# Kernel tuning notes

Measured on AMD Instinct MI355X. Metric: run time of the kernel, lower is better.

The kernel has to match this reference:

```python
import jax, jax.numpy as jnp
import numpy as np

EPS = 1e-12
B, S, H, NH, L, F = 8, 512, 768, 12, 12, 3072
V, TV, P = 21128, 2, 512
DH = H // NH


def layer_norm(x, g, b):
    m = jnp.mean(x, axis=-1, keepdims=True)
    v = jnp.var(x, axis=-1, keepdims=True)
    return g * (x - m) / jnp.sqrt(v + EPS) + b


def setup_inputs() -> dict:
    key = jax.random.key(0)
    ks = iter(jax.random.split(key, 40))
    r = lambda shape: (jax.random.normal(next(ks), shape, jnp.float32) * 0.02)
    inp = {
        "input_ids": jax.random.randint(next(ks), (B, S), 0, V, jnp.int32),
        "segment_ids": jax.random.randint(next(ks), (B, S), 0, TV, jnp.int32),
        "attention_mask": jnp.ones((B, 1, 1, S), jnp.float32),
        "tok_emb": r((V, H)),
        "pos_emb": r((P, H)),
        "type_emb": r((TV, H)),
        "emb_g": jnp.ones((H,), jnp.float32),
        "emb_b": jnp.zeros((H,), jnp.float32),
        # stacked per-layer params [L, ...]
        "Wq": r((L, H, H)), "bq": jnp.zeros((L, H), jnp.float32),
        "Wk": r((L, H, H)), "bk": jnp.zeros((L, H), jnp.float32),
        "Wv": r((L, H, H)), "bv": jnp.zeros((L, H), jnp.float32),
        "Wao": r((L, H, H)), "bao": jnp.zeros((L, H), jnp.float32),
        "ln1_g": jnp.ones((L, H), jnp.float32), "ln1_b": jnp.zeros((L, H), jnp.float32),
        "Wi": r((L, H, F)), "bi": jnp.zeros((L, F), jnp.float32),
        "Wio": r((L, F, H)), "bio": jnp.zeros((L, H), jnp.float32),
        "ln2_g": jnp.ones((L, H), jnp.float32), "ln2_b": jnp.zeros((L, H), jnp.float32),
    }
    return inp


def reference(input_ids, segment_ids, attention_mask,
              tok_emb, pos_emb, type_emb, emb_g, emb_b,
              Wq, bq, Wk, bk, Wv, bv, Wao, bao, ln1_g, ln1_b,
              Wi, bi, Wio, bio, ln2_g, ln2_b):
    # ---- embedding: token + type + position, then LayerNorm ----
    x = tok_emb[input_ids] + type_emb[segment_ids] + pos_emb[None, :S, :]
    x = layer_norm(x, emb_g, emb_b)  # [B,S,H]

    mask_add = (1.0 - attention_mask) * -10000.0  # [B,1,1,S]
    scale = 1.0 / jnp.sqrt(jnp.asarray(DH, x.dtype))

    def split_heads(t):  # [B,S,H] -> [B,NH,S,DH]
        return t.reshape(B, S, NH, DH).transpose(0, 2, 1, 3)

    for l in range(Wq.shape[0]):
        q = split_heads(x @ Wq[l] + bq[l])
        k = split_heads(x @ Wk[l] + bk[l])
        v = split_heads(x @ Wv[l] + bv[l])
        score = jnp.einsum("bhqd,bhkd->bhqk", q, k) * scale + mask_add
        attn = jax.nn.softmax(score, axis=-1)
        ctx = jnp.einsum("bhqk,bhkd->bhqd", attn, v)
        ctx = ctx.transpose(0, 2, 1, 3).reshape(B, S, H)
        # attention output: dense + residual + LN
        attn_out = layer_norm(ctx @ Wao[l] + bao[l] + x, ln1_g[l], ln1_b[l])
        # FFN: dense-gelu-dense + residual + LN (exact erf gelu as in tf.keras)
        h = jax.nn.gelu(attn_out @ Wi[l] + bi[l], approximate=False)
        x = layer_norm(h @ Wio[l] + bio[l] + attn_out, ln2_g[l], ln2_b[l])

    return x  # sequence output [B,S,H]
```

## Files before the change

kernel.cpp:

```cpp
#include <hip/hip_runtime.h>
#include <math.h>

static constexpr int Bc = 8;
static constexpr int Sc = 512;
static constexpr int Hc = 768;
static constexpr int NHc = 12;
static constexpr int Lc = 12;
static constexpr int Fc = 3072;
static constexpr int DHc = 64;
static constexpr int NTOK = Bc * Sc;
static constexpr int QKVN = 3 * Hc;

static constexpr size_t W_QKV_OFF = 0;
static constexpr size_t W_AO_OFF  = 1769472;
static constexpr size_t W_I_OFF   = 2359296;
static constexpr size_t W_IO_OFF  = 4718592;
static constexpr size_t LW        = 7077888;

typedef _Float16 h16x8 __attribute__((ext_vector_type(8)));
typedef float f32x4 __attribute__((ext_vector_type(4)));
typedef unsigned short us4 __attribute__((ext_vector_type(4)));
typedef unsigned short us8 __attribute__((ext_vector_type(8)));
typedef unsigned int u32x4 __attribute__((ext_vector_type(4)));

__device__ __forceinline__ unsigned short f2h(float f) {
    _Float16 h = (_Float16)f;
    return __builtin_bit_cast(unsigned short, h);
}

#define AS1 __attribute__((address_space(1)))
#define AS3 __attribute__((address_space(3)))
__device__ __forceinline__ void gld_lds16(const void* g, void* l) {
    __builtin_amdgcn_global_load_lds((const AS1 void*)g, (AS3 void*)l, 16, 0, 0);
}

__global__ __launch_bounds__(256) void prep_kernel(
    const float* __restrict__ Wq, const float* __restrict__ Wk,
    const float* __restrict__ Wv, const float* __restrict__ Wao,
    const float* __restrict__ Wi, const float* __restrict__ Wio,
    const float* __restrict__ bq, const float* __restrict__ bk,
    const float* __restrict__ bv, unsigned short* __restrict__ WALL,
    float* __restrict__ BALL)
{
    int t = blockIdx.x, l = blockIdx.y;
    int tid = threadIdx.x;

    if (t >= 1728) {
        int idx = (t - 1728) * 256 + tid;
        float v = (idx < 768) ? bq[l * Hc + idx]
                : (idx < 1536) ? bk[l * Hc + idx - 768]
                               : bv[l * Hc + idx - 1536];
        BALL[(size_t)l * QKVN + idx] = v;
        return;
    }

    const float* src;
    unsigned short* dst;
    int K, N, ntn, local;
    if (t < 576) {
        int mat = t / 144; local = t % 144;
        K = 768; N = 768; ntn = 12;
        src = (mat == 0 ? Wq : mat == 1 ? Wk : mat == 2 ? Wv : Wao) + (size_t)l * 589824;
        dst = WALL + (size_t)l * LW + (mat < 3 ? (size_t)mat * 589824 : W_AO_OFF);
    } else if (t < 1152) {
        local = t - 576; K = 768; N = 3072; ntn = 48;
        src = Wi + (size_t)l * 2359296;
        dst = WALL + (size_t)l * LW + W_I_OFF;
    } else {
        local = t - 1152; K = 3072; N = 768; ntn = 12;
        src = Wio + (size_t)l * 2359296;
        dst = WALL + (size_t)l * LW + W_IO_OFF;
    }
    int n0 = (local % ntn) * 64, k0 = (local / ntn) * 64;

    __shared__ float tl[64][65];
    int tx = tid & 15, ty = tid >> 4;
#pragma unroll
    for (int j = 0; j < 4; j++) {
        int k = ty + j * 16;
        float4 v = *(const float4*)(src + (size_t)(k0 + k) * N + n0 + tx * 4);
        tl[k][tx * 4 + 0] = v.x; tl[k][tx * 4 + 1] = v.y;
        tl[k][tx * 4 + 2] = v.z; tl[k][tx * 4 + 3] = v.w;
    }
    __syncthreads();
#pragma unroll
    for (int q = 0; q < 2; q++) {
        int chunk = q * 256 + tid;
        int row = chunk >> 3, c = chunk & 7;
        us8 o;
#pragma unroll
        for (int j = 0; j < 8; j++) o[j] = f2h(tl[c * 8 + j][row]);
        *(us8*)(dst + (size_t)(n0 + row) * K + k0 + c * 8) = o;
    }
}

__global__ __launch_bounds__(256) void embed_ln_kernel(
    const int* __restrict__ ids, const int* __restrict__ seg,
    const float* __restrict__ tok, const float* __restrict__ typ,
    const float* __restrict__ pos, const float* __restrict__ g,
    const float* __restrict__ b, float* __restrict__ outf,
    unsigned short* __restrict__ outb)
{
    int t = blockIdx.x;
    int si = t % Sc;
    int id = ids[t], sg = seg[t];
    const float* tp = tok + (size_t)id * Hc;
    const float* yp = typ + (size_t)sg * Hc;
    const float* pp = pos + (size_t)si * Hc;

    float e[3];
    float s = 0.f, s2 = 0.f;
#pragma unroll
    for (int j = 0; j < 3; j++) {
        int h = threadIdx.x + j * 256;
        float v = tp[h] + yp[h] + pp[h];
        e[j] = v; s += v; s2 += v * v;
    }
    __shared__ float red[8];
#pragma unroll
    for (int o = 32; o > 0; o >>= 1) { s += __shfl_xor(s, o); s2 += __shfl_xor(s2, o); }
    int lane = threadIdx.x & 63, wid = threadIdx.x >> 6;
    if (lane == 0) { red[wid] = s; red[4 + wid] = s2; }
    __syncthreads();
    if (threadIdx.x == 0) {
        red[0] = red[0] + red[1] + red[2] + red[3];
        red[4] = red[4] + red[5] + red[6] + red[7];
    }
    __syncthreads();
    float mean = red[0] * (1.0f / Hc);
    float var  = red[4] * (1.0f / Hc) - mean * mean;
    float rstd = rsqrtf(var + 1e-12f);
    float* op = outf + (size_t)t * Hc;
    unsigned short* ob = outb + (size_t)t * Hc;
#pragma unroll
    for (int j = 0; j < 3; j++) {
        int h = threadIdx.x + j * 256;
        float v = g[h] * (e[j] - mean) * rstd + b[h];
        op[h] = v;
        ob[h] = f2h(v);
    }
}

__global__ __launch_bounds__(256) void add_ln_kernel(
    const unsigned short* __restrict__ tin, const float* __restrict__ res,
    const float* __restrict__ g, const float* __restrict__ b,
    float* __restrict__ outf, unsigned short* __restrict__ outb)
{
    int t = blockIdx.x;
    const unsigned short* ip = tin + (size_t)t * Hc;
    const float* rp = res + (size_t)t * Hc;

    float e[3];
    float s = 0.f, s2 = 0.f;
#pragma unroll
    for (int j = 0; j < 3; j++) {
        int h = threadIdx.x + j * 256;
        float v = (float)__builtin_bit_cast(_Float16, ip[h]) + rp[h];
        e[j] = v; s += v; s2 += v * v;
    }
    __shared__ float red[8];
#pragma unroll
    for (int o = 32; o > 0; o >>= 1) { s += __shfl_xor(s, o); s2 += __shfl_xor(s2, o); }
    int lane = threadIdx.x & 63, wid = threadIdx.x >> 6;
    if (lane == 0) { red[wid] = s; red[4 + wid] = s2; }
    __syncthreads();
    if (threadIdx.x == 0) {
        red[0] = red[0] + red[1] + red[2] + red[3];
        red[4] = red[4] + red[5] + red[6] + red[7];
    }
    __syncthreads();
    float mean = red[0] * (1.0f / Hc);
    float var  = red[4] * (1.0f / Hc) - mean * mean;
    float rstd = rsqrtf(var + 1e-12f);
    float* op = outf + (size_t)t * Hc;
    unsigned short* ob = outb + (size_t)t * Hc;
#pragma unroll
    for (int j = 0; j < 3; j++) {
        int h = threadIdx.x + j * 256;
        float v = g[h] * (e[j] - mean) * rstd + b[h];
        op[h] = v;
        ob[h] = f2h(v);
    }
}

__global__ __launch_bounds__(256) void add_ln2f_kernel(
    const float* __restrict__ t0, const float* __restrict__ t1,
    const float* __restrict__ res, const float* __restrict__ g,
    const float* __restrict__ b, float* __restrict__ outf,
    unsigned short* __restrict__ outb)
{
    int t = blockIdx.x;
    const float* i0 = t0 + (size_t)t * Hc;
    const float* i1 = t1 + (size_t)t * Hc;
    const float* rp = res + (size_t)t * Hc;

    float e[3];
    float s = 0.f, s2 = 0.f;
#pragma unroll
    for (int j = 0; j < 3; j++) {
        int h = threadIdx.x + j * 256;
        float v = i0[h] + i1[h] + rp[h];
        e[j] = v; s += v; s2 += v * v;
    }
    __shared__ float red[8];
#pragma unroll
    for (int o = 32; o > 0; o >>= 1) { s += __shfl_xor(s, o); s2 += __shfl_xor(s2, o); }
    int lane = threadIdx.x & 63, wid = threadIdx.x >> 6;
    if (lane == 0) { red[wid] = s; red[4 + wid] = s2; }
    __syncthreads();
    if (threadIdx.x == 0) {
        red[0] = red[0] + red[1] + red[2] + red[3];
        red[4] = red[4] + red[5] + red[6] + red[7];
    }
    __syncthreads();
    float mean = red[0] * (1.0f / Hc);
    float var  = red[4] * (1.0f / Hc) - mean * mean;
    float rstd = rsqrtf(var + 1e-12f);
    float* op = outf + (size_t)t * Hc;
    unsigned short* ob = outb + (size_t)t * Hc;
#pragma unroll
    for (int j = 0; j < 3; j++) {
        int h = threadIdx.x + j * 256;
        float v = g[h] * (e[j] - mean) * rstd + b[h];
        op[h] = v;
        ob[h] = f2h(v);
    }
}

template <int OUT>
__global__ __launch_bounds__(256) void gemm_mfma(
    const unsigned short* __restrict__ A,
    const unsigned short* __restrict__ Bt,
    const float* __restrict__ bias,
    unsigned short* __restrict__ Cb,
    unsigned short* __restrict__ VTp,
    float* __restrict__ Cf,
    int M, int N, int K, int kspan)
{
    __shared__ __align__(16) unsigned short As[128 * 64];
    __shared__ __align__(16) unsigned short Bs[128 * 64];

    int tid = threadIdx.x;
    int l = tid & 63, w = tid >> 6;
    int m0 = blockIdx.x * 128, n0 = blockIdx.y * 128;
    int lr = l & 15;
    int kg = l >> 4;
    int wr = (w >> 1) * 64, wc = (w & 1) * 64;
    int lx = lr & 7;
    int kbeg = blockIdx.z * kspan;

    f32x4 acc[4][4] = {};

    for (int k0 = kbeg; k0 < kbeg + kspan; k0 += 64) {
#pragma unroll
        for (int p = 0; p < 4; p++) {
            int i = p * 256 + w * 64 + l;
            int row = i >> 3;
            int slot = (i & 7) ^ (row & 7);
            const unsigned short* ga = A + (size_t)(m0 + row) * K + k0 + slot * 8;
            const unsigned short* gb = Bt + (size_t)(n0 + row) * K + k0 + slot * 8;
            unsigned short* la = As + (size_t)(p * 256 + w * 64) * 8;
            unsigned short* lb = Bs + (size_t)(p * 256 + w * 64) * 8;
            gld_lds16(ga, la);
            gld_lds16(gb, lb);
        }
        asm volatile("s_waitcnt vmcnt(0)" ::: "memory");
        __syncthreads();

#pragma unroll
        for (int kh = 0; kh < 2; kh++) {
            h16x8 av[4], bv[4];
#pragma unroll
            for (int f = 0; f < 4; f++) {
                int sl = (kh * 4 + kg) ^ lx;
                av[f] = *(const h16x8*)(As + (wr + f * 16 + lr) * 64 + sl * 8);
                bv[f] = *(const h16x8*)(Bs + (wc + f * 16 + lr) * 64 + sl * 8);
            }
#pragma unroll
            for (int i = 0; i < 4; i++)
#pragma unroll
                for (int j = 0; j < 4; j++)
                    acc[i][j] = __builtin_amdgcn_mfma_f32_16x16x32_f16(
                        av[i], bv[j], acc[i][j], 0, 0, 0);
        }
        __syncthreads();
    }

#pragma unroll
    for (int i = 0; i < 4; i++) {
        int rbase = m0 + wr + i * 16 + kg * 4;
#pragma unroll
        for (int j = 0; j < 4; j++) {
            int col = n0 + wc + j * 16 + lr;
            float bcol = (OUT == 4 && blockIdx.z > 0) ? 0.f : bias[col];
            if (OUT == 3 && col >= 1536) {
                int vcol = col - 1536;
                int hh = vcol >> 6, d = vcol & 63;
                int bbb = rbase >> 9, s0 = rbase & 511;
                us4 ob;
#pragma unroll
                for (int r = 0; r < 4; r++) ob[r] = f2h(acc[i][j][r] + bcol);
                *(us4*)(VTp + ((((size_t)bbb * NHc + hh) * DHc + d) << 9) + s0) = ob;
            } else if (OUT == 4) {
                float* op = Cf + (size_t)blockIdx.z * M * N;
#pragma unroll
                for (int r = 0; r < 4; r++)
                    op[(size_t)(rbase + r) * N + col] = acc[i][j][r] + bcol;
            } else {
                int ldc = (OUT == 3) ? 1536 : N;
#pragma unroll
                for (int r = 0; r < 4; r++) {
                    float v = acc[i][j][r] + bcol;
                    if (OUT == 1) v = 0.5f * v * (1.0f + erff(v * 0.70710678118654752f));
                    Cb[(size_t)(rbase + r) * ldc + col] = f2h(v);
                }
            }
        }
    }
}

__global__ __launch_bounds__(256) void attn_mfma(
    const unsigned short* __restrict__ QK, const unsigned short* __restrict__ VT,
    const float* __restrict__ mask, unsigned short* __restrict__ O)
{
    const int LD = 1536;
    __shared__ __align__(16) unsigned short Ks[64 * 64];
    __shared__ __align__(16) unsigned short Vt[64 * 64];
    __shared__ float Ml[64];

    int tid = threadIdx.x;
    int l = tid & 63, w = tid >> 6;
    int g = l >> 4, c = l & 15;
    int q0 = blockIdx.x * 64;
    int h = blockIdx.y, bb = blockIdx.z;

    const size_t rowQ = (size_t)(bb * Sc + q0 + w * 16 + c) * LD + h * DHc;
    h16x8 qv[2];
    qv[0] = *(const h16x8*)(QK + rowQ + 8 * g);
    qv[1] = *(const h16x8*)(QK + rowQ + 32 + 8 * g);

    float m_run = -1e30f, l_run = 0.f;
    f32x4 acc_o[4] = {};
    const float scale = 0.125f;

    for (int kt = 0; kt < Sc; kt += 64) {
        const unsigned short* Kgb = QK + (size_t)(bb * Sc + kt) * LD + Hc + h * DHc;
#pragma unroll
        for (int p = 0; p < 2; p++) {
            int i = p * 256 + tid;
            int row = i >> 3;
            int slot = (i & 7) ^ (row & 7);
            gld_lds16(Kgb + (size_t)row * LD + slot * 8, Ks + (size_t)(p * 256 + w * 64) * 8);
        }
        const unsigned short* Vg = VT + (((size_t)bb * NHc + h) * DHc << 9) + kt;
#pragma unroll
        for (int p = 0; p < 2; p++) {
            int i = p * 256 + tid;
            int row = i >> 3;
            int slot = (i & 7) ^ (row & 7);
            gld_lds16(Vg + ((size_t)row << 9) + slot * 8, Vt + (size_t)(p * 256 + w * 64) * 8);
        }
        if (tid < 64) Ml[tid] = (1.0f - mask[bb * Sc + kt + tid]) * -10000.0f;
        asm volatile("s_waitcnt vmcnt(0)" ::: "memory");
        __syncthreads();

        f32x4 s[4] = {};
#pragma unroll
        for (int kh = 0; kh < 2; kh++) {
#pragma unroll
            for (int f = 0; f < 4; f++) {
                int row = f * 16 + c;
                h16x8 av = *(const h16x8*)(Ks + row * 64 + (((kh * 4 + g) ^ (row & 7)) * 8));
                s[f] = __builtin_amdgcn_mfma_f32_16x16x32_f16(av, qv[kh], s[f], 0, 0, 0);
            }
        }

        f32x4 mv[4];
#pragma unroll
        for (int f = 0; f < 4; f++) mv[f] = *(const f32x4*)&Ml[f * 16 + 4 * g];
        float mx = -1e30f;
#pragma unroll
        for (int f = 0; f < 4; f++)
#pragma unroll
            for (int r = 0; r < 4; r++) {
                float sv = s[f][r] * scale + mv[f][r];
                s[f][r] = sv;
                mx = fmaxf(mx, sv);
            }
        mx = fmaxf(mx, __shfl_xor(mx, 16));
        mx = fmaxf(mx, __shfl_xor(mx, 32));
        float mn = fmaxf(m_run, mx);
        float fs = __expf(m_run - mn);
        m_run = mn;
        float ps = 0.f;
        f32x4 p[4];
#pragma unroll
        for (int f = 0; f < 4; f++)
#pragma unroll
            for (int r = 0; r < 4; r++) {
                float pv = __expf(s[f][r] - mn);
                p[f][r] = pv;
                ps += pv;
            }
        ps += __shfl_xor(ps, 16);
        ps += __shfl_xor(ps, 32);
        l_run = l_run * fs + ps;
#pragma unroll
        for (int fm = 0; fm < 4; fm++)
#pragma unroll
            for (int r = 0; r < 4; r++) acc_o[fm][r] *= fs;

        unsigned pk[4][2];
#pragma unroll
        for (int f = 0; f < 4; f++)
#pragma unroll
            for (int rp = 0; rp < 2; rp++)
                pk[f][rp] = ((unsigned)f2h(p[f][2 * rp + 1]) << 16) | f2h(p[f][2 * rp]);

#pragma unroll
        for (int kh = 0; kh < 2; kh++) {
            u32x4 bw;
#pragma unroll
            for (int t = 0; t < 4; t++) {
                int srcl = (2 * ((l >> 4) & 1) + (t >> 1)) * 16 + c;
                unsigned lo = __shfl(pk[2 * kh][t & 1], srcl);
                unsigned hi = __shfl(pk[2 * kh + 1][t & 1], srcl);
                bw[t] = (g & 2) ? hi : lo;
            }
            h16x8 bfrag = __builtin_bit_cast(h16x8, bw);
#pragma unroll
            for (int fm = 0; fm < 4; fm++) {
                int row = fm * 16 + c;
                h16x8 av = *(const h16x8*)(Vt + row * 64 + (((kh * 4 + g) ^ (row & 7)) * 8));
                acc_o[fm] = __builtin_amdgcn_mfma_f32_16x16x32_f16(av, bfrag, acc_o[fm], 0, 0, 0);
            }
        }
        __syncthreads();
    }

    float rl = 1.0f / l_run;
    size_t tokrow = (size_t)(bb * Sc + q0 + w * 16 + c) * Hc + h * DHc;
#pragma unroll
    for (int fm = 0; fm < 4; fm++) {
        us4 ob;
#pragma unroll
        for (int r = 0; r < 4; r++) ob[r] = f2h(acc_o[fm][r] * rl);
        *(us4*)(O + tokrow + fm * 16 + 4 * g) = ob;
    }
}

extern "C" void kernel_launch(void* const* d_in, const int* in_sizes, int n_in,
                              void* d_out, int out_size, void* d_ws, size_t ws_size,
                              hipStream_t stream)
{
    const int*   input_ids      = (const int*)  d_in[0];
    const int*   segment_ids    = (const int*)  d_in[1];
    const float* attention_mask = (const float*)d_in[2];
    const float* tok_emb = (const float*)d_in[3];
    const float* pos_emb = (const float*)d_in[4];
    const float* type_emb= (const float*)d_in[5];
    const float* emb_g   = (const float*)d_in[6];
    const float* emb_b   = (const float*)d_in[7];
    const float* Wq  = (const float*)d_in[8];  const float* bq  = (const float*)d_in[9];
    const float* Wk  = (const float*)d_in[10]; const float* bk  = (const float*)d_in[11];
    const float* Wv  = (const float*)d_in[12]; const float* bv  = (const float*)d_in[13];
    const float* Wao = (const float*)d_in[14]; const float* bao = (const float*)d_in[15];
    const float* ln1_g = (const float*)d_in[16]; const float* ln1_b = (const float*)d_in[17];
    const float* Wi  = (const float*)d_in[18]; const float* bi  = (const float*)d_in[19];
    const float* Wio = (const float*)d_in[20]; const float* bio = (const float*)d_in[21];
    const float* ln2_g = (const float*)d_in[22]; const float* ln2_b = (const float*)d_in[23];

    float* out = (float*)d_out;

    const size_t NT = (size_t)NTOK * Hc;
    float* Xf   = (float*)d_ws;
    float* XAf  = Xf + NT;
    float* Tf01 = XAf + NT;
    float* BALL = Tf01 + 2 * NT;
    unsigned short* QKb = (unsigned short*)(BALL + (size_t)Lc * QKVN);
    unsigned short* VT  = QKb + (size_t)NTOK * 1536;
    unsigned short* Xb  = VT + NT;
    unsigned short* XAb = Xb + NT;
    unsigned short* Cb  = XAb + NT;
    unsigned short* Tb  = Cb + NT;
    unsigned short* Hb  = Tb + NT;
    unsigned short* WALL = Hb + (size_t)NTOK * Fc;

    prep_kernel<<<dim3(1737, Lc), 256, 0, stream>>>(Wq, Wk, Wv, Wao, Wi, Wio,
                                                    bq, bk, bv, WALL, BALL);

    embed_ln_kernel<<<NTOK, 256, 0, stream>>>(input_ids, segment_ids, tok_emb,
                                              type_emb, pos_emb, emb_g, emb_b, Xf, Xb);

    dim3 gQKV(NTOK / 128, QKVN / 128);
    dim3 gH(NTOK / 128, Hc / 128);
    dim3 gF(NTOK / 128, Fc / 128);
    dim3 gH2(NTOK / 128, Hc / 128, 2);
    dim3 gA(Sc / 64, NHc, Bc);

    for (int l = 0; l < Lc; l++) {
        const unsigned short* WqkvT = WALL + (size_t)l * LW + W_QKV_OFF;
        const unsigned short* WaoT  = WALL + (size_t)l * LW + W_AO_OFF;
        const unsigned short* WiT   = WALL + (size_t)l * LW + W_I_OFF;
        const unsigned short* WioT  = WALL + (size_t)l * LW + W_IO_OFF;
        const float* bqkv = BALL + (size_t)l * QKVN;

        gemm_mfma<3><<<gQKV, 256, 0, stream>>>(Xb, WqkvT, bqkv, QKb, VT, nullptr,
                                               NTOK, QKVN, Hc, Hc);
        attn_mfma<<<gA, 256, 0, stream>>>(QKb, VT, attention_mask, Cb);

        gemm_mfma<2><<<gH, 256, 0, stream>>>(Cb, WaoT, bao + (size_t)l * Hc, Tb, nullptr,
                                             nullptr, NTOK, Hc, Hc, Hc);
        add_ln_kernel<<<NTOK, 256, 0, stream>>>(Tb, Xf, ln1_g + (size_t)l * Hc,
                                                ln1_b + (size_t)l * Hc, XAf, XAb);

        gemm_mfma<1><<<gF, 256, 0, stream>>>(XAb, WiT, bi + (size_t)l * Fc, Hb, nullptr,
                                             nullptr, NTOK, Fc, Hc, Hc);
        gemm_mfma<4><<<gH2, 256, 0, stream>>>(Hb, WioT, bio + (size_t)l * Hc, nullptr,
                                              nullptr, Tf01, NTOK, Hc, Fc, Fc / 2);
        float* xout = (l == Lc - 1) ? out : Xf;
        add_ln2f_kernel<<<NTOK, 256, 0, stream>>>(Tf01, Tf01 + NT, XAf,
                                                  ln2_g + (size_t)l * Hc,
                                                  ln2_b + (size_t)l * Hc, xout, Xb);
    }
}
```

Measured before the change: 2.070 ms.

## Double-buffer GEMM LDS staging and make weight prep loop over K strips

The MFMA GEMM now double-buffers its A/B LDS tiles, issuing the global-to-LDS loads for the next K step before waiting only on the current tile, so memory latency overlaps with compute. The weight transpose/convert prep kernel is restructured so each block walks 12 consecutive 64-wide K tiles of one column strip, prefetching the next tile into registers. This uses far fewer blocks and hides load latency. Doubling the LDS footprint to 64KB per GEMM block may lower occupancy.

```diff
diff --git a/kernel.cpp b/kernel.cpp
--- a/kernel.cpp
+++ b/kernel.cpp
@@ -45,8 +45,8 @@
     int t = blockIdx.x, l = blockIdx.y;
     int tid = threadIdx.x;
 
-    if (t >= 1728) {
-        int idx = (t - 1728) * 256 + tid;
+    if (t >= 144) {
+        int idx = (t - 144) * 256 + tid;
         float v = (idx < 768) ? bq[l * Hc + idx]
                 : (idx < 1536) ? bk[l * Hc + idx - 768]
                                : bv[l * Hc + idx - 1536];
@@ -56,41 +56,57 @@
 
     const float* src;
     unsigned short* dst;
-    int K, N, ntn, local;
-    if (t < 576) {
-        int mat = t / 144; local = t % 144;
-        K = 768; N = 768; ntn = 12;
+    int K, N, n0, kbase;
+    if (t < 48) {
+        int mat = t / 12, strip = t % 12;
+        K = 768; N = 768; n0 = strip * 64; kbase = 0;
         src = (mat == 0 ? Wq : mat == 1 ? Wk : mat == 2 ? Wv : Wao) + (size_t)l * 589824;
         dst = WALL + (size_t)l * LW + (mat < 3 ? (size_t)mat * 589824 : W_AO_OFF);
-    } else if (t < 1152) {
-        local = t - 576; K = 768; N = 3072; ntn = 48;
+    } else if (t < 96) {
+        int strip = t - 48;
+        K = 768; N = 3072; n0 = strip * 64; kbase = 0;
         src = Wi + (size_t)l * 2359296;
         dst = WALL + (size_t)l * LW + W_I_OFF;
     } else {
-        local = t - 1152; K = 3072; N = 768; ntn = 12;
+        int local = t - 96;
+        int strip = local >> 2, kc = local & 3;
+        K = 3072; N = 768; n0 = strip * 64; kbase = kc * 768;
         src = Wio + (size_t)l * 2359296;
         dst = WALL + (size_t)l * LW + W_IO_OFF;
     }
-    int n0 = (local % ntn) * 64, k0 = (local / ntn) * 64;
 
     __shared__ float tl[64][65];
     int tx = tid & 15, ty = tid >> 4;
-#pragma unroll
-    for (int j = 0; j < 4; j++) {
-        int k = ty + j * 16;
-        float4 v = *(const float4*)(src + (size_t)(k0 + k) * N + n0 + tx * 4);
-        tl[k][tx * 4 + 0] = v.x; tl[k][tx * 4 + 1] = v.y;
-        tl[k][tx * 4 + 2] = v.z; tl[k][tx * 4 + 3] = v.w;
-    }
-    __syncthreads();
-#pragma unroll
-    for (int q = 0; q < 2; q++) {
-        int chunk = q * 256 + tid;
-        int row = chunk >> 3, c = chunk & 7;
-        us8 o;
-#pragma unroll
-        for (int j = 0; j < 8; j++) o[j] = f2h(tl[c * 8 + j][row]);
-        *(us8*)(dst + (size_t)(n0 + row) * K + k0 + c * 8) = o;
+
+    float4 v[4];
+#pragma unroll
+    for (int j = 0; j < 4; j++)
+        v[j] = *(const float4*)(src + (size_t)(kbase + ty + j * 16) * N + n0 + tx * 4);
+
+    for (int it = 0; it < 12; it++) {
+        int k0 = kbase + it * 64;
+#pragma unroll
+        for (int j = 0; j < 4; j++) {
+            int k = ty + j * 16;
+            tl[k][tx * 4 + 0] = v[j].x; tl[k][tx * 4 + 1] = v[j].y;
+            tl[k][tx * 4 + 2] = v[j].z; tl[k][tx * 4 + 3] = v[j].w;
+        }
+        __syncthreads();
+        if (it + 1 < 12) {
+#pragma unroll
+            for (int j = 0; j < 4; j++)
+                v[j] = *(const float4*)(src + (size_t)(k0 + 64 + ty + j * 16) * N + n0 + tx * 4);
+        }
+#pragma unroll
+        for (int q = 0; q < 2; q++) {
+            int chunk = q * 256 + tid;
+            int row = chunk >> 3, c = chunk & 7;
+            us8 o;
+#pragma unroll
+            for (int j = 0; j < 8; j++) o[j] = f2h(tl[c * 8 + j][row]);
+            *(us8*)(dst + (size_t)(n0 + row) * K + k0 + c * 8) = o;
+        }
+        __syncthreads();
     }
 }
 
@@ -237,8 +253,8 @@
     float* __restrict__ Cf,
     int M, int N, int K, int kspan)
 {
-    __shared__ __align__(16) unsigned short As[128 * 64];
-    __shared__ __align__(16) unsigned short Bs[128 * 64];
+    __shared__ __align__(16) unsigned short As[2][128 * 64];
+    __shared__ __align__(16) unsigned short Bs[2][128 * 64];
 
     int tid = threadIdx.x;
     int l = tid & 63, w = tid >> 6;
@@ -248,33 +264,47 @@
     int wr = (w >> 1) * 64, wc = (w & 1) * 64;
     int lx = lr & 7;
     int kbeg = blockIdx.z * kspan;
+    int nk = kspan / 64;
 
     f32x4 acc[4][4] = {};
 
-    for (int k0 = kbeg; k0 < kbeg + kspan; k0 += 64) {
+    auto stage = [&](int buf, int k0) {
+        unsigned short* as = &As[buf][0];
+        unsigned short* bs = &Bs[buf][0];
 #pragma unroll
         for (int p = 0; p < 4; p++) {
             int i = p * 256 + w * 64 + l;
             int row = i >> 3;
             int slot = (i & 7) ^ (row & 7);
-            const unsigned short* ga = A + (size_t)(m0 + row) * K + k0 + slot * 8;
-            const unsigned short* gb = Bt + (size_t)(n0 + row) * K + k0 + slot * 8;
-            unsigned short* la = As + (size_t)(p * 256 + w * 64) * 8;
-            unsigned short* lb = Bs + (size_t)(p * 256 + w * 64) * 8;
-            gld_lds16(ga, la);
-            gld_lds16(gb, lb);
-        }
-        asm volatile("s_waitcnt vmcnt(0)" ::: "memory");
+            gld_lds16(A + (size_t)(m0 + row) * K + k0 + slot * 8,
+                      as + (size_t)(p * 256 + w * 64) * 8);
+            gld_lds16(Bt + (size_t)(n0 + row) * K + k0 + slot * 8,
+                      bs + (size_t)(p * 256 + w * 64) * 8);
+        }
+    };
+
+    stage(0, kbeg);
+
+    for (int t = 0; t < nk; t++) {
+        int cur = t & 1;
+        if (t + 1 < nk) {
+            stage(cur ^ 1, kbeg + (t + 1) * 64);
+            asm volatile("s_waitcnt vmcnt(8)" ::: "memory");
+        } else {
+            asm volatile("s_waitcnt vmcnt(0)" ::: "memory");
+        }
         __syncthreads();
 
+        const unsigned short* as = &As[cur][0];
+        const unsigned short* bs = &Bs[cur][0];
 #pragma unroll
         for (int kh = 0; kh < 2; kh++) {
             h16x8 av[4], bv[4];
 #pragma unroll
             for (int f = 0; f < 4; f++) {
                 int sl = (kh * 4 + kg) ^ lx;
-                av[f] = *(const h16x8*)(As + (wr + f * 16 + lr) * 64 + sl * 8);
-                bv[f] = *(const h16x8*)(Bs + (wc + f * 16 + lr) * 64 + sl * 8);
+                av[f] = *(const h16x8*)(as + (wr + f * 16 + lr) * 64 + sl * 8);
+                bv[f] = *(const h16x8*)(bs + (wc + f * 16 + lr) * 64 + sl * 8);
             }
 #pragma unroll
             for (int i = 0; i < 4; i++)
@@ -486,8 +516,8 @@
     unsigned short* Hb  = Tb + NT;
     unsigned short* WALL = Hb + (size_t)NTOK * Fc;
 
-    prep_kernel<<<dim3(1737, Lc), 256, 0, stream>>>(Wq, Wk, Wv, Wao, Wi, Wio,
-                                                    bq, bk, bv, WALL, BALL);
+    prep_kernel<<<dim3(153, Lc), 256, 0, stream>>>(Wq, Wk, Wv, Wao, Wi, Wio,
+                                                   bq, bk, bv, WALL, BALL);
 
     embed_ln_kernel<<<NTOK, 256, 0, stream>>>(input_ids, segment_ids, tok_emb,
                                               type_emb, pos_emb, emb_g, emb_b, Xf, Xb);
```

After: 2.371 ms. +14.5%, slower.

## Split-K the attention-output GEMM and vectorize LayerNorm kernels to 192 threads

Applied to the files above, without the earlier changes.

The attention-output projection now uses the split-K GEMM variant (two K halves written as fp32 partials), and its residual LayerNorm reuses the two-partial add_ln2f kernel. This doubles the block count of that 768x768 GEMM for better CU occupancy, but it writes fp32 partials instead of a half-precision result, which adds memory traffic. Separately, the embedding and LayerNorm kernels are rewritten to use 192 threads, each handling one float4, with a single-barrier reduction. This cuts the loop, scalar loads and an extra sync in those kernels.

```diff
diff --git a/kernel.cpp b/kernel.cpp
--- a/kernel.cpp
+++ b/kernel.cpp
@@ -26,6 +26,9 @@
 __device__ __forceinline__ unsigned short f2h(float f) {
     _Float16 h = (_Float16)f;
     return __builtin_bit_cast(unsigned short, h);
+}
+__device__ __forceinline__ float h2f(unsigned short u) {
+    return (float)__builtin_bit_cast(_Float16, u);
 }
 
 #define AS1 __attribute__((address_space(1)))
@@ -94,7 +97,23 @@
     }
 }
 
-__global__ __launch_bounds__(256) void embed_ln_kernel(
+__device__ __forceinline__ void ln_stats192(float4 v, float& mean, float& rstd) {
+    float s = v.x + v.y + v.z + v.w;
+    float s2 = v.x * v.x + v.y * v.y + v.z * v.z + v.w * v.w;
+#pragma unroll
+    for (int o = 32; o > 0; o >>= 1) { s += __shfl_xor(s, o); s2 += __shfl_xor(s2, o); }
+    __shared__ float red[6];
+    int lane = threadIdx.x & 63, wid = threadIdx.x >> 6;
+    if (lane == 0) { red[wid] = s; red[3 + wid] = s2; }
+    __syncthreads();
+    float ts  = red[0] + red[1] + red[2];
+    float ts2 = red[3] + red[4] + red[5];
+    mean = ts * (1.0f / Hc);
+    float var = ts2 * (1.0f / Hc) - mean * mean;
+    rstd = rsqrtf(var + 1e-12f);
+}
+
+__global__ __launch_bounds__(192) void embed_ln_kernel(
     const int* __restrict__ ids, const int* __restrict__ seg,
     const float* __restrict__ tok, const float* __restrict__ typ,
     const float* __restrict__ pos, const float* __restrict__ g,
@@ -104,127 +123,52 @@
     int t = blockIdx.x;
     int si = t % Sc;
     int id = ids[t], sg = seg[t];
-    const float* tp = tok + (size_t)id * Hc;
-    const float* yp = typ + (size_t)sg * Hc;
-    const float* pp = pos + (size_t)si * Hc;
-
-    float e[3];
-    float s = 0.f, s2 = 0.f;
-#pragma unroll
-    for (int j = 0; j < 3; j++) {
-        int h = threadIdx.x + j * 256;
-        float v = tp[h] + yp[h] + pp[h];
-        e[j] = v; s += v; s2 += v * v;
-    }
-    __shared__ float red[8];
-#pragma unroll
-    for (int o = 32; o > 0; o >>= 1) { s += __shfl_xor(s, o); s2 += __shfl_xor(s2, o); }
-    int lane = threadIdx.x & 63, wid = threadIdx.x >> 6;
-    if (lane == 0) { red[wid] = s; red[4 + wid] = s2; }
-    __syncthreads();
-    if (threadIdx.x == 0) {
-        red[0] = red[0] + red[1] + red[2] + red[3];
-        red[4] = red[4] + red[5] + red[6] + red[7];
-    }
-    __syncthreads();
-    float mean = red[0] * (1.0f / Hc);
-    float var  = red[4] * (1.0f / Hc) - mean * mean;
-    float rstd = rsqrtf(var + 1e-12f);
-    float* op = outf + (size_t)t * Hc;
-    unsigned short* ob = outb + (size_t)t * Hc;
-#pragma unroll
-    for (int j = 0; j < 3; j++) {
-        int h = threadIdx.x + j * 256;
-        float v = g[h] * (e[j] - mean) * rstd + b[h];
-        op[h] = v;
-        ob[h] = f2h(v);
-    }
-}
-
-__global__ __launch_bounds__(256) void add_ln_kernel(
-    const unsigned short* __restrict__ tin, const float* __restrict__ res,
-    const float* __restrict__ g, const float* __restrict__ b,
-    float* __restrict__ outf, unsigned short* __restrict__ outb)
-{
-    int t = blockIdx.x;
-    const unsigned short* ip = tin + (size_t)t * Hc;
-    const float* rp = res + (size_t)t * Hc;
-
-    float e[3];
-    float s = 0.f, s2 = 0.f;
-#pragma unroll
-    for (int j = 0; j < 3; j++) {
-        int h = threadIdx.x + j * 256;
-        float v = (float)__builtin_bit_cast(_Float16, ip[h]) + rp[h];
-        e[j] = v; s += v; s2 += v * v;
-    }
-    __shared__ float red[8];
-#pragma unroll
-    for (int o = 32; o > 0; o >>= 1) { s += __shfl_xor(s, o); s2 += __shfl_xor(s2, o); }
-    int lane = threadIdx.x & 63, wid = threadIdx.x >> 6;
-    if (lane == 0) { red[wid] = s; red[4 + wid] = s2; }
-    __syncthreads();
-    if (threadIdx.x == 0) {
-        red[0] = red[0] + red[1] + red[2] + red[3];
-        red[4] = red[4] + red[5] + red[6] + red[7];
-    }
-    __syncthreads();
-    float mean = red[0] * (1.0f / Hc);
-    float var  = red[4] * (1.0f / Hc) - mean * mean;
-    float rstd = rsqrtf(var + 1e-12f);
-    float* op = outf + (size_t)t * Hc;
-    unsigned short* ob = outb + (size_t)t * Hc;
-#pragma unroll
-    for (int j = 0; j < 3; j++) {
-        int h = threadIdx.x + j * 256;
-        float v = g[h] * (e[j] - mean) * rstd + b[h];
-        op[h] = v;
-        ob[h] = f2h(v);
-    }
-}
-
-__global__ __launch_bounds__(256) void add_ln2f_kernel(
+    int i = threadIdx.x;
+
+    float4 tv = *(const float4*)(tok + (size_t)id * Hc + 4 * i);
+    float4 yv = *(const float4*)(typ + (size_t)sg * Hc + 4 * i);
+    float4 pv = *(const float4*)(pos + (size_t)si * Hc + 4 * i);
+    float4 v = make_float4(tv.x + yv.x + pv.x, tv.y + yv.y + pv.y,
+                           tv.z + yv.z + pv.z, tv.w + yv.w + pv.w);
+    float mean, rstd;
+    ln_stats192(v, mean, rstd);
+
+    float4 gv = *(const float4*)(g + 4 * i);
+    float4 bv = *(const float4*)(b + 4 * i);
+    float4 o = make_float4(gv.x * (v.x - mean) * rstd + bv.x,
+                           gv.y * (v.y - mean) * rstd + bv.y,
+                           gv.z * (v.z - mean) * rstd + bv.z,
+                           gv.w * (v.w - mean) * rstd + bv.w);
+    *(float4*)(outf + (size_t)t * Hc + 4 * i) = o;
+    us4 ob; ob[0] = f2h(o.x); ob[1] = f2h(o.y); ob[2] = f2h(o.z); ob[3] = f2h(o.w);
+    *(us4*)(outb + (size_t)t * Hc + 4 * i) = ob;
+}
+
+__global__ __launch_bounds__(192) void add_ln2f_kernel(
     const float* __restrict__ t0, const float* __restrict__ t1,
     const float* __restrict__ res, const float* __restrict__ g,
     const float* __restrict__ b, float* __restrict__ outf,
     unsigned short* __restrict__ outb)
 {
     int t = blockIdx.x;
-    const float* i0 = t0 + (size_t)t * Hc;
-    const float* i1 = t1 + (size_t)t * Hc;
-    const float* rp = res + (size_t)t * Hc;
-
-    float e[3];
-    float s = 0.f, s2 = 0.f;
-#pragma unroll
-    for (int j = 0; j < 3; j++) {
-        int h = threadIdx.x + j * 256;
-        float v = i0[h] + i1[h] + rp[h];
-        e[j] = v; s += v; s2 += v * v;
-    }
-    __shared__ float red[8];
-#pragma unroll
-    for (int o = 32; o > 0; o >>= 1) { s += __shfl_xor(s, o); s2 += __shfl_xor(s2, o); }
-    int lane = threadIdx.x & 63, wid = threadIdx.x >> 6;
-    if (lane == 0) { red[wid] = s; red[4 + wid] = s2; }
-    __syncthreads();
-    if (threadIdx.x == 0) {
-        red[0] = red[0] + red[1] + red[2] + red[3];
-        red[4] = red[4] + red[5] + red[6] + red[7];
-    }
-    __syncthreads();
-    float mean = red[0] * (1.0f / Hc);
-    float var  = red[4] * (1.0f / Hc) - mean * mean;
-    float rstd = rsqrtf(var + 1e-12f);
-    float* op = outf + (size_t)t * Hc;
-    unsigned short* ob = outb + (size_t)t * Hc;
-#pragma unroll
-    for (int j = 0; j < 3; j++) {
-        int h = threadIdx.x + j * 256;
-        float v = g[h] * (e[j] - mean) * rstd + b[h];
-        op[h] = v;
-        ob[h] = f2h(v);
-    }
+    int i = threadIdx.x;
+    float4 a = *(const float4*)(t0 + (size_t)t * Hc + 4 * i);
+    float4 c = *(const float4*)(t1 + (size_t)t * Hc + 4 * i);
+    float4 r = *(const float4*)(res + (size_t)t * Hc + 4 * i);
+    float4 v = make_float4(a.x + c.x + r.x, a.y + c.y + r.y,
+                           a.z + c.z + r.z, a.w + c.w + r.w);
+    float mean, rstd;
+    ln_stats192(v, mean, rstd);
+
+    float4 gv = *(const float4*)(g + 4 * i);
+    float4 bv = *(const float4*)(b + 4 * i);
+    float4 o = make_float4(gv.x * (v.x - mean) * rstd + bv.x,
+                           gv.y * (v.y - mean) * rstd + bv.y,
+                           gv.z * (v.z - mean) * rstd + bv.z,
+                           gv.w * (v.w - mean) * rstd + bv.w);
+    *(float4*)(outf + (size_t)t * Hc + 4 * i) = o;
+    us4 ob; ob[0] = f2h(o.x); ob[1] = f2h(o.y); ob[2] = f2h(o.z); ob[3] = f2h(o.w);
+    *(us4*)(outb + (size_t)t * Hc + 4 * i) = ob;
 }
 
 template <int OUT>
@@ -482,18 +426,16 @@
     unsigned short* Xb  = VT + NT;
     unsigned short* XAb = Xb + NT;
     unsigned short* Cb  = XAb + NT;
-    unsigned short* Tb  = Cb + NT;
-    unsigned short* Hb  = Tb + NT;
+    unsigned short* Hb  = Cb + NT;
     unsigned short* WALL = Hb + (size_t)NTOK * Fc;
 
     prep_kernel<<<dim3(1737, Lc), 256, 0, stream>>>(Wq, Wk, Wv, Wao, Wi, Wio,
                                                     bq, bk, bv, WALL, BALL);
 
-    embed_ln_kernel<<<NTOK, 256, 0, stream>>>(input_ids, segment_ids, tok_emb,
+    embed_ln_kernel<<<NTOK, 192, 0, stream>>>(input_ids, segment_ids, tok_emb,
                                               type_emb, pos_emb, emb_g, emb_b, Xf, Xb);
 
     dim3 gQKV(NTOK / 128, QKVN / 128);
-    dim3 gH(NTOK / 128, Hc / 128);
     dim3 gF(NTOK / 128, Fc / 128);
     dim3 gH2(NTOK / 128, Hc / 128, 2);
     dim3 gA(Sc / 64, NHc, Bc);
@@ -509,17 +451,18 @@
                                                NTOK, QKVN, Hc, Hc);
         attn_mfma<<<gA, 256, 0, stream>>>(QKb, VT, attention_mask, Cb);
 
-        gemm_mfma<2><<<gH, 256, 0, stream>>>(Cb, WaoT, bao + (size_t)l * Hc, Tb, nullptr,
-                                             nullptr, NTOK, Hc, Hc, Hc);
-        add_ln_kernel<<<NTOK, 256, 0, stream>>>(Tb, Xf, ln1_g + (size_t)l * Hc,
-                                                ln1_b + (size_t)l * Hc, XAf, XAb);
+        gemm_mfma<4><<<gH2, 256, 0, stream>>>(Cb, WaoT, bao + (size_t)l * Hc, nullptr,
+                                              nullptr, Tf01, NTOK, Hc, Hc, Hc / 2);
+        add_ln2f_kernel<<<NTOK, 192, 0, stream>>>(Tf01, Tf01 + NT, Xf,
+                                                  ln1_g + (size_t)l * Hc,
+                                                  ln1_b + (size_t)l * Hc, XAf, XAb);
 
         gemm_mfma<1><<<gF, 256, 0, stream>>>(XAb, WiT, bi + (size_t)l * Fc, Hb, nullptr,
                                              nullptr, NTOK, Fc, Hc, Hc);
         gemm_mfma<4><<<gH2, 256, 0, stream>>>(Hb, WioT, bio + (size_t)l * Hc, nullptr,
                                               nullptr, Tf01, NTOK, Hc, Fc, Fc / 2);
         float* xout = (l == Lc - 1) ? out : Xf;
-        add_ln2f_kernel<<<NTOK, 256, 0, stream>>>(Tf01, Tf01 + NT, XAf,
+        add_ln2f_kernel<<<NTOK, 192, 0, stream>>>(Tf01, Tf01 + NT, XAf,
                                                   ln2_g + (size_t)l * Hc,
                                                   ln2_b + (size_t)l * Hc, xout, Xb);
     }
```

After: 2.040 ms. Within noise of the previous version (-1.4%).
